# Optimization experiments

Hardware: AMD Instinct MI355X
Metric: run time of the kernel (lower is better)

Reference implementation:

```python
import jax, jax.numpy as jnp
import numpy as np

N, E, B, H, F = 20000, 400000, 200, 10, 78
HID = H * F  # 780
SEQ, VOC, EMB, NF, KS = 1000, 26, 128, 32, 8
CONV_OUT = SEQ - KS + 1  # 993


def setup_inputs() -> dict:
    key = jax.random.key(0)
    ks = jax.random.split(key, 40)
    g = lambda i, shape, s=0.05: jax.random.normal(ks[i], shape, jnp.float32) * s
    inp = {
        "x": jax.random.normal(ks[0], (N, F), jnp.float32),
        "edge_index": jax.random.randint(ks[1], (2, E), 0, N),
        "batch": jnp.sort(jax.random.randint(ks[2], (N,), 0, B)),
        "target": jax.random.randint(ks[3], (B, SEQ), 0, VOC),
        # GATConv(78 -> 78, heads=10)
        "gat_W": g(4, (F, HID)),
        "gat_a_src": g(5, (H, F)),
        "gat_a_dst": g(6, (H, F)),
        "gat_b": g(7, (HID,)),
        # GCNConv(780 -> 780)
        "gcn_W": g(8, (HID, HID)),
        "gcn_b": g(9, (HID,)),
        # graph MLP head
        "fcg1_W": g(10, (HID, 1500)), "fcg1_b": g(11, (1500,)),
        "fcg2_W": g(12, (1500, 128)), "fcg2_b": g(13, (128,)),
        # protein branch
        "emb": g(14, (VOC, EMB)),
        "cW": g(15, (NF, EMB, KS)), "cb": g(16, (NF,)),
        "fxt_W": g(17, (NF * CONV_OUT, 128)), "fxt_b": g(18, (128,)),
        # fusion MLP
        "f1_W": g(19, (256, 1024)), "f1_b": g(20, (1024,)),
        "f2_W": g(21, (1024, 512)), "f2_b": g(22, (512,)),
        "f3_W": g(23, (512, 256)), "f3_b": g(24, (256,)),
        "f4_W": g(25, (256, 128)), "f4_b": g(26, (128,)),
        "o_W": g(27, (128, 1)), "o_b": g(28, (1,)),
    }
    return inp


def _graph_branch(x, edge_index, batch, gat_W, gat_a_src, gat_a_dst, gat_b,
                  gcn_W, gcn_b, fcg1_W, fcg1_b, fcg2_W, fcg2_b):
    n = x.shape[0]
    loops = jnp.arange(n)
    src = jnp.concatenate([edge_index[0], loops])  # add self loops (PyG default)
    dst = jnp.concatenate([edge_index[1], loops])
    # --- GATConv ---
    h = (x @ gat_W).reshape(n, H, F)  # [N,H,F]
    a_s = jnp.einsum("nhf,hf->nh", h, gat_a_src)
    a_d = jnp.einsum("nhf,hf->nh", h, gat_a_dst)
    e = jax.nn.leaky_relu(a_s[src] + a_d[dst], 0.2)  # [Etot,H]
    m = jax.ops.segment_max(e, dst, num_segments=n)
    ex = jnp.exp(e - m[dst])
    den = jax.ops.segment_sum(ex, dst, num_segments=n)
    alpha = ex / den[dst]
    agg = jax.ops.segment_sum(h[src] * alpha[:, :, None], dst, num_segments=n)
    x1 = jax.nn.relu(agg.reshape(n, HID) + gat_b)
    # --- GCNConv (sym norm with self loops) ---
    deg = jax.ops.segment_sum(jnp.ones_like(dst, jnp.float32), dst, num_segments=n)
    dinv = jax.lax.rsqrt(jnp.maximum(deg, 1.0))
    norm = dinv[src] * dinv[dst]
    h2 = x1 @ gcn_W
    x2 = jax.ops.segment_sum(h2[src] * norm[:, None], dst, num_segments=n) + gcn_b
    x2 = jax.nn.relu(x2)
    # --- global add pool + MLP ---
    xg = jax.ops.segment_sum(x2, batch, num_segments=B)
    xg = jax.nn.relu(xg @ fcg1_W + fcg1_b)  # dropout = identity (eval)
    return xg @ fcg2_W + fcg2_b


def _protein_branch(target, emb, cW, cb, fxt_W, fxt_b):
    et = emb[target]  # [B,SEQ,EMB]
    c = jax.lax.conv_general_dilated(
        et.transpose(0, 2, 1), cW, (1,), "VALID",
        dimension_numbers=("NCH", "OIH", "NCH"))  # [B,NF,993]
    c = c + cb[None, :, None]
    return c.reshape(c.shape[0], NF * CONV_OUT) @ fxt_W + fxt_b


def reference(x, edge_index, batch, target, gat_W, gat_a_src, gat_a_dst, gat_b,
              gcn_W, gcn_b, fcg1_W, fcg1_b, fcg2_W, fcg2_b, emb, cW, cb,
              fxt_W, fxt_b, f1_W, f1_b, f2_W, f2_b, f3_W, f3_b, f4_W, f4_b,
              o_W, o_b):
    xg = _graph_branch(x, edge_index, batch, gat_W, gat_a_src, gat_a_dst, gat_b,
                       gcn_W, gcn_b, fcg1_W, fcg1_b, fcg2_W, fcg2_b)
    xt = _protein_branch(target, emb, cW, cb, fxt_W, fxt_b)
    xc = jnp.concatenate([xg, xt], axis=1)  # [B,256]
    xc = jax.nn.relu(xc @ f1_W + f1_b)
    xc = jax.nn.relu(xc @ f2_W + f2_b)
    xc = jax.nn.relu(xc @ f3_W + f3_b)
    xc = jax.nn.relu(xc @ f4_W + f4_b)
    return xc @ o_W + o_b  # [B,1]
```

## Files before the change

### kernel.cpp

```cpp
#include <hip/hip_runtime.h>
#include <hip/hip_bf16.h>
#include <math.h>

typedef __hip_bfloat16 bf16;
typedef __attribute__((ext_vector_type(8))) short short8v;
typedef __attribute__((ext_vector_type(4))) float float4v;

#define NODES 20000
#define EDG   400000
#define ETOT  (EDG + NODES)
#define GB    200
#define HEADS 10
#define FD    78
#define HIDD  780
#define SEQL  1000
#define VOCS  26
#define EMBD  128
#define NFC   32
#define KSZ   8
#define COUT  993
#define KFXT  (NFC * COUT)

#define MPAD  20096
#define NPADB 896
#define KP1   96
#define KP2   800
#define HP    784


__device__ __forceinline__ float us2f(unsigned short u) {
  unsigned int i = ((unsigned int)u) << 16; float f; __builtin_memcpy(&f, &i, 4); return f;
}
__device__ __forceinline__ float b2f(bf16 v) { return __bfloat162float(v); }
__device__ __forceinline__ float ldany(const void* p, size_t i, int m) {
  if (m) return ((const float*)p)[i];
  return b2f(((const bf16*)p)[i]);
}
__device__ __forceinline__ bool nanf_(float v) { return v != v; }
__device__ __forceinline__ unsigned short f2us(float v) {
  bf16 b = __float2bfloat16(v); unsigned short u; __builtin_memcpy(&u, &b, 2); return u;
}

__global__ void k_detect(const void* x, int* diag) {
  int t = threadIdx.x;
  const unsigned short* u = (const unsigned short*)x;
  int hit = 0;
  for (int i = t; i < 4096; i += 256) {
    float v = us2f(u[i]);
    if (nanf_(v) || fabsf(v) > 1e6f) hit = 1;
  }
  if (hit) diag[1] = 1;
}

__global__ void k_pad_x(const void* x, bf16* xpad, const int* diag) {
  int idx = blockIdx.x * 256 + threadIdx.x;
  if (idx >= MPAD * KP1) return;
  int mode = diag[1];
  int m = idx / KP1, k = idx % KP1;
  float v = (m < NODES && k < FD) ? ldany(x, (size_t)m * FD + k, mode) : 0.f;
  xpad[idx] = __float2bfloat16(v);
}

__global__ void k_tr_gatw(const void* gw, bf16* Wt, const int* diag) {
  int idx = blockIdx.x * 256 + threadIdx.x;
  if (idx >= NPADB * KP1) return;
  int mode = diag[1];
  int n = idx / KP1, k = idx % KP1;
  float v = (n < HIDD && k < FD) ? ldany(gw, (size_t)k * HIDD + n, mode) : 0.f;
  Wt[idx] = __float2bfloat16(v);
}

__global__ void k_tr_gcnw(const void* gw, bf16* Wt, const int* diag) {
  int idx = blockIdx.x * 256 + threadIdx.x;
  if (idx >= NPADB * KP2) return;
  int mode = diag[1];
  int n = idx / KP2, k = idx % KP2;
  float v = (n < HIDD && k < HIDD) ? ldany(gw, (size_t)k * HIDD + n, mode) : 0.f;
  Wt[idx] = __float2bfloat16(v);
}

__global__ void k_zero_x1pad(bf16* x1p) {
  int i = blockIdx.x * 256 + threadIdx.x;
  if (i < (MPAD - NODES) * KP2)
    x1p[(size_t)NODES * KP2 + i] = __float2bfloat16(0.f);
}

#define MT 128
#define NT 128
#define BK 32
#define LP 40
__global__ __launch_bounds__(256) void k_gemm_mfma(const bf16* A, int lda,
                                                   const bf16* Bt, int ldb,
                                                   bf16* C, int ldc, int Ncap,
                                                   int M, int Kp) {
  __shared__ __align__(16) bf16 As[MT * LP];
  __shared__ __align__(16) bf16 Bs[NT * LP];
  int t = threadIdx.x;
  int lane = t & 63, w = t >> 6;
  int wr = (w >> 1) * 64, wc = (w & 1) * 64;
  int quad = lane >> 4, mr = lane & 15;
  int m0 = blockIdx.y * MT, n0 = blockIdx.x * NT;
  float4v acc[4][4];
#pragma unroll
  for (int i = 0; i < 4; ++i)
#pragma unroll
    for (int j = 0; j < 4; ++j) acc[i][j] = (float4v){0.f, 0.f, 0.f, 0.f};

  for (int kc = 0; kc < Kp; kc += BK) {
#pragma unroll
    for (int i = 0; i < 4; ++i) {
      int c = t + i * 256;
      int row = c >> 3, col = (c & 7) * 4;
      *(uint2*)&As[row * LP + col] =
          *(const uint2*)&A[(size_t)(m0 + row) * lda + kc + col];
      *(uint2*)&Bs[row * LP + col] =
          *(const uint2*)&Bt[(size_t)(n0 + row) * ldb + kc + col];
    }
    __syncthreads();
    short8v af[4], bfr[4];
#pragma unroll
    for (int i = 0; i < 4; ++i)
      af[i] = *(const short8v*)&As[(wr + i * 16 + mr) * LP + quad * 8];
#pragma unroll
    for (int j = 0; j < 4; ++j)
      bfr[j] = *(const short8v*)&Bs[(wc + j * 16 + mr) * LP + quad * 8];
#pragma unroll
    for (int i = 0; i < 4; ++i)
#pragma unroll
      for (int j = 0; j < 4; ++j)
        acc[i][j] = __builtin_amdgcn_mfma_f32_16x16x32_bf16(af[i], bfr[j], acc[i][j], 0, 0, 0);
    __syncthreads();
  }
#pragma unroll
  for (int i = 0; i < 4; ++i) {
    int gm0 = m0 + wr + i * 16 + quad * 4;
#pragma unroll
    for (int j = 0; j < 4; ++j) {
      int gn = n0 + wc + j * 16 + mr;
      if (gn >= Ncap) continue;
#pragma unroll
      for (int r = 0; r < 4; ++r) {
        int gm = gm0 + r;
        if (gm < M) C[(size_t)gm * ldc + gn] = __float2bfloat16(acc[i][j][r]);
      }
    }
  }
}

#define MLP_NT 64
#define MLP_BK 32
#define MLP_MT 208
#define MLP_LP 40
__global__ __launch_bounds__(256) void k_mlp_mfma(const void* A, int lda, const void* Bw,
                                                  const void* bias, float* out, int ostride,
                                                  int ooff, int M, int Nn, int K,
                                                  int ksplit, int aRelu, int aBf16,
                                                  const int* diag) {
  __shared__ __align__(16) bf16 As[MLP_MT * MLP_LP];
  __shared__ __align__(16) bf16 Bs[MLP_NT * MLP_LP];
  int mode = diag[1];
  int t = threadIdx.x;
  int lane = t & 63, w = t >> 6;
  int quad = lane >> 4, mr = lane & 15;
  int n0 = blockIdx.x * MLP_NT;
  int kz = blockIdx.y;
  int nchunks = (K + MLP_BK - 1) / MLP_BK;
  int cpk = (nchunks + ksplit - 1) / ksplit;
  int c0 = kz * cpk, c1 = c0 + cpk;
  if (c1 > nchunks) c1 = nchunks;
  float4v acc[13];
#pragma unroll
  for (int i = 0; i < 13; ++i) acc[i] = (float4v){0.f, 0.f, 0.f, 0.f};

  for (int c = c0; c < c1; ++c) {
    int k0 = c * MLP_BK;
    if (aBf16) {
      const bf16* Ab = (const bf16*)A;
      for (int e = t; e < MLP_MT * 4; e += 256) {
        int row = e >> 2, c8 = (e & 3) * 8;
        int gk = k0 + c8;
        if (row < M && gk + 7 < K) {
          *(uint4*)&As[row * MLP_LP + c8] = *(const uint4*)&Ab[(size_t)row * lda + gk];
        } else {
#pragma unroll
          for (int kk = 0; kk < 8; ++kk) {
            float v = (row < M && gk + kk < K) ? b2f(Ab[(size_t)row * lda + gk + kk]) : 0.f;
            As[row * MLP_LP + c8 + kk] = __float2bfloat16(v);
          }
        }
      }
    } else {
      const float* Af = (const float*)A;
      for (int e = t; e < MLP_MT * 8; e += 256) {
        int row = e >> 3, c4 = (e & 7) * 4;
        int gk = k0 + c4;
        float4 v4 = {0.f, 0.f, 0.f, 0.f};
        if (row < M) {
          if (gk + 3 < K) {
            v4 = *(const float4*)&Af[(size_t)row * lda + gk];
          } else {
            v4.x = (gk + 0 < K) ? Af[(size_t)row * lda + gk + 0] : 0.f;
            v4.y = (gk + 1 < K) ? Af[(size_t)row * lda + gk + 1] : 0.f;
            v4.z = (gk + 2 < K) ? Af[(size_t)row * lda + gk + 2] : 0.f;
            v4.w = (gk + 3 < K) ? Af[(size_t)row * lda + gk + 3] : 0.f;
          }
        }
        if (aRelu) {
          v4.x = fmaxf(v4.x, 0.f); v4.y = fmaxf(v4.y, 0.f);
          v4.z = fmaxf(v4.z, 0.f); v4.w = fmaxf(v4.w, 0.f);
        }
        bf16* dst = &As[row * MLP_LP + c4];
        dst[0] = __float2bfloat16(v4.x); dst[1] = __float2bfloat16(v4.y);
        dst[2] = __float2bfloat16(v4.z); dst[3] = __float2bfloat16(v4.w);
      }
    }
    for (int e = t; e < MLP_NT * MLP_BK; e += 256) {
      int k = e >> 6, col = e & 63;
      int gk = k0 + k, gn = n0 + col;
      float v = (gn < Nn && gk < K) ? ldany(Bw, (size_t)gk * Nn + gn, mode) : 0.f;
      Bs[col * MLP_LP + k] = __float2bfloat16(v);
    }
    __syncthreads();
    short8v bf = *(const short8v*)&Bs[(w * 16 + mr) * MLP_LP + quad * 8];
#pragma unroll
    for (int i = 0; i < 13; ++i) {
      short8v af = *(const short8v*)&As[(i * 16 + mr) * MLP_LP + quad * 8];
      acc[i] = __builtin_amdgcn_mfma_f32_16x16x32_bf16(af, bf, acc[i], 0, 0, 0);
    }
    __syncthreads();
  }
  int gn = n0 + w * 16 + mr;
  if (gn >= Nn) return;
  float bs = (kz == 0) ? ldany(bias, gn, mode) : 0.f;
#pragma unroll
  for (int i = 0; i < 13; ++i) {
    int gm0 = i * 16 + quad * 4;
#pragma unroll
    for (int r = 0; r < 4; ++r) {
      int gm = gm0 + r;
      if (gm >= M) break;
      float v = acc[i][r] + bs;
      float* op = &out[(size_t)gm * ostride + ooff + gn];
      if (ksplit == 1) *op = v;
      else atomicAdd(op, v);
    }
  }
}

__global__ void k_prep_ws(const void* gat_W, const void* a_src, const void* a_dst,
                          float* Ws, float* Wd, const int* diag) {
  int idx = blockIdx.x * 256 + threadIdx.x;
  if (idx >= FD * HEADS) return;
  int mode = diag[1];
  int k = idx / HEADS, hd = idx % HEADS;
  float s = 0.f, d = 0.f;
  for (int f = 0; f < FD; ++f) {
    float w = ldany(gat_W, (size_t)k * HIDD + hd * FD + f, mode);
    s += w * ldany(a_src, (size_t)hd * FD + f, mode);
    d += w * ldany(a_dst, (size_t)hd * FD + f, mode);
  }
  Ws[k * HEADS + hd] = s;
  Wd[k * HEADS + hd] = d;
}

__global__ void k_prep_mtab(const void* emb, const void* cW, float* Mtab, const int* diag) {
  int idx = blockIdx.x * 256 + threadIdx.x;
  if (idx >= NFC * KSZ * VOCS) return;
  int mode = diag[1];
  int o = idx / (KSZ * VOCS);
  int r = idx % (KSZ * VOCS);
  int k = r / VOCS, v = r % VOCS;
  float acc = 0.f;
  for (int i = 0; i < EMBD; ++i)
    acc += ldany(emb, (size_t)v * EMBD + i, mode) * ldany(cW, ((size_t)o * EMBD + i) * KSZ + k, mode);
  Mtab[idx] = acc;
}

__global__ __launch_bounds__(256) void k_asd(const void* x, const float* Ws, const float* Wd,
                                             float* a_s, float* a_d, const int* diag) {
  __shared__ unsigned short xs[256 * FD];
  __shared__ float ws_sh[FD * HEADS], wd_sh[FD * HEADS];
  int mode = diag[1];
  int nb = blockIdx.x * 256, t = threadIdx.x;
  for (int e = t; e < FD * HEADS; e += 256) { ws_sh[e] = Ws[e]; wd_sh[e] = Wd[e]; }
  for (int e = t; e < 256 * FD; e += 256) {
    int r = e / FD, c = e % FD;
    int gn = nb + r;
    float xv = (gn < NODES) ? ldany(x, (size_t)gn * FD + c, mode) : 0.f;
    xs[e] = f2us(xv);
  }
  __syncthreads();
  int n = nb + t;
  if (n >= NODES) return;
  float as[HEADS], ad[HEADS];
#pragma unroll
  for (int hd = 0; hd < HEADS; ++hd) { as[hd] = 0.f; ad[hd] = 0.f; }
  for (int f = 0; f < FD; ++f) {
    float xv = us2f(xs[t * FD + f]);
#pragma unroll
    for (int hd = 0; hd < HEADS; ++hd) {
      as[hd] += xv * ws_sh[f * HEADS + hd];
      ad[hd] += xv * wd_sh[f * HEADS + hd];
    }
  }
#pragma unroll
  for (int hd = 0; hd < HEADS; ++hd) {
    a_s[n * HEADS + hd] = as[hd];
    a_d[n * HEADS + hd] = ad[hd];
  }
}

__global__ void k_count(const int* ei, int* cnt, int* diag) {
  int e = blockIdx.x * 256 + threadIdx.x;
  if (e >= ETOT) return;
  int d = (e < EDG) ? ei[EDG + e] : (e - EDG);
  if ((unsigned)d >= NODES) { atomicOr(diag, 8192); d = 0; }
  atomicAdd(&cnt[d], 1);
}

__global__ __launch_bounds__(1024) void k_scan(const int* cnt, int* rowstart) {
  __shared__ int sh[1024];
  __shared__ int carry;
  int t = threadIdx.x;
  if (t == 0) carry = 0;
  __syncthreads();
  for (int c = 0; c < (NODES + 1023) / 1024; ++c) {
    int i = c * 1024 + t;
    int v = (i < NODES) ? cnt[i] : 0;
    sh[t] = v;
    __syncthreads();
    for (int off = 1; off < 1024; off <<= 1) {
      int add = (t >= off) ? sh[t - off] : 0;
      __syncthreads();
      sh[t] += add;
      __syncthreads();
    }
    int tot = sh[1023];
    int excl = sh[t] - v + carry;
    if (i < NODES) rowstart[i] = excl;
    __syncthreads();
    if (t == 0) carry += tot;
    __syncthreads();
  }
  if (t == 0) rowstart[NODES] = carry;
}

__global__ void k_dinv(const int* cnt, float* dinv) {
  int n = blockIdx.x * 256 + threadIdx.x;
  if (n >= NODES) return;
  int d = cnt[n];
  dinv[n] = rsqrtf((float)(d > 0 ? d : 1));
}

__global__ void k_scatter(const int* ei, const int* rowstart, int* cur, int* es_src,
                          int* diag) {
  int e = blockIdx.x * 256 + threadIdx.x;
  if (e >= ETOT) return;
  int s, d;
  if (e < EDG) { s = ei[e]; d = ei[EDG + e]; } else { s = e - EDG; d = s; }
  if ((unsigned)d >= NODES) { atomicOr(diag, 8192); d = 0; }
  if ((unsigned)s >= NODES) { atomicOr(diag, 8192); s = 0; }
  int pos = rowstart[d] + atomicAdd(&cur[d], 1);
  if ((unsigned)pos < (unsigned)ETOT) es_src[pos] = s;
  else atomicOr(diag, 1);
}

__global__ void k_csrchk(const int* cnt, const int* cur, const int* rowst, int* diag) {
  int n = blockIdx.x * 256 + threadIdx.x;
  if (n < NODES && cur[n] != cnt[n]) atomicOr(diag, 1);
  if (n == 0 && rowst[NODES] != ETOT) atomicOr(diag, 1);
}

__global__ void k_bseg(const int* batch, int* bstart, int* diag) {
  int i = blockIdx.x * 256 + threadIdx.x;
  if (i >= NODES) return;
  int bi = batch[i];
  if ((unsigned)bi >= GB) { atomicOr(diag, 8192); bi = GB - 1; }
  int bp;
  if (i == 0) bp = -1;
  else {
    bp = batch[i - 1];
    if ((unsigned)bp >= GB) bp = GB - 1;
  }
  for (int b = bp + 1; b <= bi; ++b) bstart[b] = i;
  if (i == NODES - 1)
    for (int b = bi + 1; b <= GB; ++b) bstart[b] = NODES;
}

__global__ __launch_bounds__(256) void k_gat(const int* es_src, const int* rowstart,
                                             const float* a_s, const float* a_d,
                                             const bf16* h, const void* gat_b, bf16* x1,
                                             int* diag) {
  int d = blockIdx.x, t = threadIdx.x;
  __shared__ float ad_sh[HEADS], m_sh[HEADS], den_sh[HEADS];
  __shared__ float exs[256 * HEADS];
  __shared__ int ssrc[256];
  __shared__ float wred[4 * HEADS];
  int mode = diag[1];
  int start = rowstart[d], end = rowstart[d + 1];
  if (t < HEADS) ad_sh[t] = a_d[d * HEADS + t];
  __syncthreads();

  float mx[HEADS];
#pragma unroll
  for (int hd = 0; hd < HEADS; ++hd) mx[hd] = -INFINITY;
  for (int e = start + t; e < end; e += 256) {
    int s = es_src[e];
    if ((unsigned)s >= NODES) { atomicOr(diag, 1); s = 0; }
#pragma unroll
    for (int hd = 0; hd < HEADS; ++hd) {
      float v = a_s[s * HEADS + hd] + ad_sh[hd];
      v = v > 0.f ? v : 0.2f * v;
      mx[hd] = fmaxf(mx[hd], v);
    }
  }
#pragma unroll
  for (int hd = 0; hd < HEADS; ++hd)
    for (int off = 32; off; off >>= 1) mx[hd] = fmaxf(mx[hd], __shfl_down(mx[hd], off, 64));
  int w = t >> 6, lane = t & 63;
  if (lane == 0) {
#pragma unroll
    for (int hd = 0; hd < HEADS; ++hd) wred[w * HEADS + hd] = mx[hd];
  }
  __syncthreads();
  if (t < HEADS)
    m_sh[t] = fmaxf(fmaxf(wred[t], wred[HEADS + t]), fmaxf(wred[2 * HEADS + t], wred[3 * HEADS + t]));
  __syncthreads();

  float acc[4] = {0.f, 0.f, 0.f, 0.f};
  float den[HEADS];
#pragma unroll
  for (int hd = 0; hd < HEADS; ++hd) den[hd] = 0.f;
  int fb = t * 4;
  int hh[4];
#pragma unroll
  for (int k = 0; k < 4; ++k) {
    int f = fb + k;
    hh[k] = (f < HIDD) ? (f / FD) : (HEADS - 1);
  }
  for (int base = start; base < end; base += 256) {
    int ce = base + t;
    if (ce < end) {
      int s = es_src[ce];
      if ((unsigned)s >= NODES) { atomicOr(diag, 1); s = 0; }
      ssrc[t] = s;
#pragma unroll
      for (int hd = 0; hd < HEADS; ++hd) {
        float v = a_s[s * HEADS + hd] + ad_sh[hd];
        v = v > 0.f ? v : 0.2f * v;
        float ex = expf(v - m_sh[hd]);
        exs[t * HEADS + hd] = ex;
        den[hd] += ex;
      }
    }
    __syncthreads();
    int cnt2 = end - base; if (cnt2 > 256) cnt2 = 256;
    if (t < 196) {
      for (int ce2 = 0; ce2 < cnt2; ++ce2) {
        int ss = ssrc[ce2];
        uint2 u = *(const uint2*)(h + (size_t)ss * HP + fb);
        acc[0] += exs[ce2 * HEADS + hh[0]] * us2f((unsigned short)(u.x & 0xffffu));
        acc[1] += exs[ce2 * HEADS + hh[1]] * us2f((unsigned short)(u.x >> 16));
        acc[2] += exs[ce2 * HEADS + hh[2]] * us2f((unsigned short)(u.y & 0xffffu));
        acc[3] += exs[ce2 * HEADS + hh[3]] * us2f((unsigned short)(u.y >> 16));
      }
    }
    __syncthreads();
  }
#pragma unroll
  for (int hd = 0; hd < HEADS; ++hd)
    for (int off = 32; off; off >>= 1) den[hd] += __shfl_down(den[hd], off, 64);
  if (lane == 0) {
#pragma unroll
    for (int hd = 0; hd < HEADS; ++hd) wred[w * HEADS + hd] = den[hd];
  }
  __syncthreads();
  if (t < HEADS)
    den_sh[t] = wred[t] + wred[HEADS + t] + wred[2 * HEADS + t] + wred[3 * HEADS + t];
  __syncthreads();

  if (t < 196) {
    bool dn = nanf_(den_sh[hh[0]]) || nanf_(den_sh[hh[3]]);
    bool an = nanf_(acc[0]) || nanf_(acc[3]);
    if (dn) atomicOr(diag, 2);
    else if (an) atomicOr(diag, 8);
  }
  if (t < 200) {
    size_t rb = (size_t)d * KP2;
#pragma unroll
    for (int k = 0; k < 4; ++k) {
      int f = fb + k;
      float o = 0.f;
      if (f < HIDD)
        o = fmaxf(acc[k] / den_sh[hh[k]] + ldany(gat_b, f, mode), 0.f);
      x1[rb + f] = __float2bfloat16(o);
    }
  }
}

__global__ __launch_bounds__(256) void k_gcn(const int* es_src, const int* rowstart,
                                             const float* dinv, const bf16* h2,
                                             const void* gcn_b, bf16* x2b, int* diag) {
  int d = blockIdx.x, t = threadIdx.x;
  __shared__ float nrm[256];
  __shared__ int ssrc[256];
  int mode = diag[1];
  int start = rowstart[d], end = rowstart[d + 1];
  float dd = dinv[d];
  float acc[4] = {0.f, 0.f, 0.f, 0.f};
  int fb = t * 4;
  for (int base = start; base < end; base += 256) {
    int ce = base + t;
    if (ce < end) {
      int s = es_src[ce];
      if ((unsigned)s >= NODES) { atomicOr(diag, 1); s = 0; }
      ssrc[t] = s;
      nrm[t] = dinv[s] * dd;
    }
    __syncthreads();
    int cnt2 = end - base; if (cnt2 > 256) cnt2 = 256;
    if (t < 195) {
      for (int ce2 = 0; ce2 < cnt2; ++ce2) {
        int ss = ssrc[ce2];
        float nv = nrm[ce2];
        uint2 u = *(const uint2*)(h2 + (size_t)ss * HP + fb);
        acc[0] += nv * us2f((unsigned short)(u.x & 0xffffu));
        acc[1] += nv * us2f((unsigned short)(u.x >> 16));
        acc[2] += nv * us2f((unsigned short)(u.y & 0xffffu));
        acc[3] += nv * us2f((unsigned short)(u.y >> 16));
      }
    }
    __syncthreads();
  }
  if (t < 196) {
    if (t < 195 && (nanf_(acc[0]) || nanf_(acc[3]))) atomicOr(diag, 16);
    unsigned short o[4];
#pragma unroll
    for (int k = 0; k < 4; ++k) {
      int f = fb + k;
      float v = 0.f;
      if (f < HIDD) v = fmaxf(acc[k] + ldany(gcn_b, f, mode), 0.f);
      o[k] = f2us(v);
    }
    uint2 pack;
    __builtin_memcpy(&pack, o, 8);
    *(uint2*)(x2b + (size_t)d * HP + fb) = pack;
  }
}

__global__ __launch_bounds__(256) void k_pool(const bf16* x2b, const int* bstart,
                                              float* xg_pool) {
  int b = blockIdx.x, t = threadIdx.x;
  if (t >= 195) return;
  int r0 = bstart[b], r1 = bstart[b + 1];
  int fb = t * 4;
  float4 acc = {0.f, 0.f, 0.f, 0.f};
  for (int r = r0; r < r1; ++r) {
    uint2 u = *(const uint2*)(x2b + (size_t)r * HP + fb);
    acc.x += us2f((unsigned short)(u.x & 0xffffu));
    acc.y += us2f((unsigned short)(u.x >> 16));
    acc.z += us2f((unsigned short)(u.y & 0xffffu));
    acc.w += us2f((unsigned short)(u.y >> 16));
  }
  *(float4*)&xg_pool[(size_t)b * HIDD + fb] = acc;
}

__global__ __launch_bounds__(256) void k_conv(const int* target, const float* Mtab,
                                              const void* cb, bf16* c, int* diag) {
  int b = blockIdx.y, tc = blockIdx.x, t = threadIdx.x;
  __shared__ float Mt[NFC * KSZ * VOCS];
  __shared__ int tg[256 + KSZ - 1];
  int mode = diag[1];
  for (int e = t; e < NFC * KSZ * VOCS; e += 256) Mt[e] = Mtab[e];
  int tbase = tc * 256;
  for (int e = t; e < 256 + KSZ - 1; e += 256) {
    int p = tbase + e;
    int tv = (p < SEQL) ? target[b * SEQL + p] : 0;
    if ((unsigned)tv >= VOCS) { atomicOr(diag, 8192); tv = 0; }
    tg[e] = tv;
  }
  __syncthreads();
  int tt = tbase + t;
  if (tt >= COUT) return;
  float acc[NFC];
#pragma unroll
  for (int o = 0; o < NFC; ++o) acc[o] = 0.f;
#pragma unroll
  for (int k = 0; k < KSZ; ++k) {
    int v = tg[t + k];
    const float* Mk = &Mt[k * VOCS + v];
#pragma unroll
    for (int o = 0; o < NFC; ++o) acc[o] += Mk[o * KSZ * VOCS];
  }
  if (nanf_(acc[0])) atomicOr(diag, 4096);
#pragma unroll
  for (int o = 0; o < NFC; ++o)
    c[(size_t)b * KFXT + o * COUT + tt] = __float2bfloat16(acc[o] + ldany(cb, o, mode));
}

__global__ __launch_bounds__(64) void k_out(const float* xf4, const void* o_W,
                                            const void* o_b, void* outp, const int* diag) {
  int b = blockIdx.x, lane = threadIdx.x;
  int mode = diag[1];
  float a0 = fmaxf(xf4[b * 128 + lane], 0.f);
  float a1 = fmaxf(xf4[b * 128 + 64 + lane], 0.f);
  float v = a0 * ldany(o_W, lane, mode) + a1 * ldany(o_W, 64 + lane, mode);
  for (int off = 32; off; off >>= 1) v += __shfl_down(v, off, 64);
  if (lane == 0) {
    float r = v + ldany(o_b, 0, mode);
    int dg = diag[0];
    if (dg) r = 256.f * (1 + mode) + 8.f * (float)(__ffs(dg) - 1);
    else if (nanf_(r)) r = 200.f + 100.f * mode;
    if (mode) ((float*)outp)[b] = r;
    else ((bf16*)outp)[b] = __float2bfloat16(r);
  }
}

extern "C" void kernel_launch(void* const* d_in, const int* in_sizes, int n_in,
                              void* d_out, int out_size, void* d_ws, size_t ws_size,
                              hipStream_t stream) {
  const void* x       = d_in[0];
  const int*  ei      = (const int*)d_in[1];
  const int*  batch   = (const int*)d_in[2];
  const int*  target  = (const int*)d_in[3];
  const void* gat_W   = d_in[4];
  const void* a_src   = d_in[5];
  const void* a_dst   = d_in[6];
  const void* gat_b   = d_in[7];
  const void* gcn_W   = d_in[8];
  const void* gcn_b   = d_in[9];
  const void* fcg1_W  = d_in[10];
  const void* fcg1_b  = d_in[11];
  const void* fcg2_W  = d_in[12];
  const void* fcg2_b  = d_in[13];
  const void* emb     = d_in[14];
  const void* cW      = d_in[15];
  const void* cb      = d_in[16];
  const void* fxt_W   = d_in[17];
  const void* fxt_b   = d_in[18];
  const void* f1_W    = d_in[19];
  const void* f1_b    = d_in[20];
  const void* f2_W    = d_in[21];
  const void* f2_b    = d_in[22];
  const void* f3_W    = d_in[23];
  const void* f3_b    = d_in[24];
  const void* f4_W    = d_in[25];
  const void* f4_b    = d_in[26];
  const void* o_W     = d_in[27];
  const void* o_b     = d_in[28];

  char* w = (char*)d_ws;
  size_t off = 0;
  auto alloc = [&](size_t bytes) -> void* {
    void* p = w + off;
    off = (off + bytes + 255) & ~(size_t)255;
    return p;
  };
  bf16*  h_buf   = (bf16*)alloc((size_t)NODES * HP * 2);
  bf16*  x1p     = (bf16*)alloc((size_t)MPAD * KP2 * 2);
  bf16*  xpad    = (bf16*)alloc((size_t)MPAD * KP1 * 2);
  bf16*  gatWt   = (bf16*)alloc((size_t)NPADB * KP1 * 2);
  bf16*  gcnWt   = (bf16*)alloc((size_t)NPADB * KP2 * 2);
  float* a_s     = (float*)alloc((size_t)NODES * HEADS * 4);
  float* a_d     = (float*)alloc((size_t)NODES * HEADS * 4);
  float* Ws      = (float*)alloc(FD * HEADS * 4);
  float* Wd      = (float*)alloc(FD * HEADS * 4);
  float* Mtab    = (float*)alloc(NFC * KSZ * VOCS * 4);
  int*   rowst   = (int*)alloc((NODES + 1) * 4);
  float* dinv    = (float*)alloc(NODES * 4);
  int*   bstart  = (int*)alloc((GB + 1) * 4);
  bf16*  c_buf   = (bf16*)alloc((size_t)GB * KFXT * 2);
  size_t zoff = off;
  int*   cnt     = (int*)alloc(NODES * 4);
  int*   cur     = (int*)alloc(NODES * 4);
  int*   es_src  = (int*)alloc((size_t)ETOT * 4);
  float* xg_pool = (float*)alloc((size_t)GB * HIDD * 4);
  float* xg1     = (float*)alloc((size_t)GB * 1500 * 4);
  float* xc      = (float*)alloc((size_t)GB * 256 * 4);
  float* xf1     = (float*)alloc((size_t)GB * 1024 * 4);
  float* xf2     = (float*)alloc((size_t)GB * 512 * 4);
  float* xf3     = (float*)alloc((size_t)GB * 256 * 4);
  float* xf4     = (float*)alloc((size_t)GB * 128 * 4);
  int*   diag    = (int*)alloc(2 * 4);
  size_t zlen = off - zoff;

  bf16* x2b = x1p;

  hipMemsetAsync(w + zoff, 0, zlen, stream);

  k_detect<<<1, 256, 0, stream>>>(x, diag);

  k_pad_x<<<(MPAD * KP1 + 255) / 256, 256, 0, stream>>>(x, xpad, diag);
  k_tr_gatw<<<(NPADB * KP1 + 255) / 256, 256, 0, stream>>>(gat_W, gatWt, diag);
  k_tr_gcnw<<<(NPADB * KP2 + 255) / 256, 256, 0, stream>>>(gcn_W, gcnWt, diag);
  k_zero_x1pad<<<((MPAD - NODES) * KP2 + 255) / 256, 256, 0, stream>>>(x1p);

  k_prep_ws<<<(FD * HEADS + 255) / 256, 256, 0, stream>>>(gat_W, a_src, a_dst, Ws, Wd, diag);
  k_prep_mtab<<<(NFC * KSZ * VOCS + 255) / 256, 256, 0, stream>>>(emb, cW, Mtab, diag);

  k_gemm_mfma<<<dim3(NPADB / NT, MPAD / MT), 256, 0, stream>>>(
      xpad, KP1, gatWt, KP1, h_buf, HP, HP, NODES, KP1);
  k_asd<<<(NODES + 255) / 256, 256, 0, stream>>>(x, Ws, Wd, a_s, a_d, diag);

  k_count<<<(ETOT + 255) / 256, 256, 0, stream>>>(ei, cnt, diag);
  k_scan<<<1, 1024, 0, stream>>>(cnt, rowst);
  k_dinv<<<(NODES + 255) / 256, 256, 0, stream>>>(cnt, dinv);
  k_scatter<<<(ETOT + 255) / 256, 256, 0, stream>>>(ei, rowst, cur, es_src, diag);
  k_csrchk<<<(NODES + 255) / 256, 256, 0, stream>>>(cnt, cur, rowst, diag);
  k_bseg<<<(NODES + 255) / 256, 256, 0, stream>>>(batch, bstart, diag);

  k_gat<<<NODES, 256, 0, stream>>>(es_src, rowst, a_s, a_d, h_buf, gat_b, x1p, diag);

  k_gemm_mfma<<<dim3(NPADB / NT, MPAD / MT), 256, 0, stream>>>(
      x1p, KP2, gcnWt, KP2, h_buf, HP, HP, NODES, KP2);

  k_gcn<<<NODES, 256, 0, stream>>>(es_src, rowst, dinv, h_buf, gcn_b, x2b, diag);
  k_pool<<<GB, 256, 0, stream>>>(x2b, bstart, xg_pool);

  k_conv<<<dim3(4, GB), 256, 0, stream>>>(target, Mtab, cb, c_buf, diag);

  k_mlp_mfma<<<dim3(24, 4), 256, 0, stream>>>(xg_pool, HIDD, fcg1_W, fcg1_b,
                                              xg1, 1500, 0, GB, 1500, HIDD, 4, 0, 0, diag);
  k_mlp_mfma<<<dim3(2, 16), 256, 0, stream>>>(xg1, 1500, fcg2_W, fcg2_b,
                                              xc, 256, 0, GB, 128, 1500, 16, 1, 0, diag);
  k_mlp_mfma<<<dim3(2, 64), 256, 0, stream>>>(c_buf, KFXT, fxt_W, fxt_b,
                                              xc, 256, 128, GB, 128, KFXT, 64, 0, 1, diag);
  k_mlp_mfma<<<dim3(16, 4), 256, 0, stream>>>(xc, 256, f1_W, f1_b,
                                              xf1, 1024, 0, GB, 1024, 256, 4, 0, 0, diag);
  k_mlp_mfma<<<dim3(8, 8), 256, 0, stream>>>(xf1, 1024, f2_W, f2_b,
                                             xf2, 512, 0, GB, 512, 1024, 8, 1, 0, diag);
  k_mlp_mfma<<<dim3(4, 8), 256, 0, stream>>>(xf2, 512, f3_W, f3_b,
                                             xf3, 256, 0, GB, 256, 512, 8, 1, 0, diag);
  k_mlp_mfma<<<dim3(2, 8), 256, 0, stream>>>(xf3, 256, f4_W, f4_b,
                                             xf4, 128, 0, GB, 128, 256, 8, 1, 0, diag);
  k_out<<<GB, 64, 0, stream>>>(xf4, o_W, o_b, d_out, diag);
}
```

Before: 0.9996 ms.

## Split GAT into alpha pass and feature-panelled gather kernels

```diff
diff --git a/kernel.cpp b/kernel.cpp
--- a/kernel.cpp
+++ b/kernel.cpp
@@ -25,7 +25,9 @@
 #define NPADB 896
 #define KP1   96
 #define KP2   800
-#define HP    784
+#define HP    800
+#define PNL   8
+#define PF    100
 
 
 __device__ __forceinline__ float us2f(unsigned short u) {
@@ -387,142 +389,156 @@
     for (int b = bi + 1; b <= GB; ++b) bstart[b] = NODES;
 }
 
-__global__ __launch_bounds__(256) void k_gat(const int* es_src, const int* rowstart,
-                                             const float* a_s, const float* a_d,
-                                             const bf16* h, const void* gat_b, bf16* x1,
-                                             int* diag) {
-  int d = blockIdx.x, t = threadIdx.x;
-  __shared__ float ad_sh[HEADS], m_sh[HEADS], den_sh[HEADS];
-  __shared__ float exs[256 * HEADS];
-  __shared__ int ssrc[256];
-  __shared__ float wred[4 * HEADS];
-  int mode = diag[1];
-  int start = rowstart[d], end = rowstart[d + 1];
-  if (t < HEADS) ad_sh[t] = a_d[d * HEADS + t];
-  __syncthreads();
-
+__global__ __launch_bounds__(64) void k_alpha(const int* es_src, const int* rowst,
+                                              const float* a_s, const float* a_d,
+                                              float* alpha, int* diag) {
+  int d = blockIdx.x, lane = threadIdx.x;
+  int start = rowst[d], end = rowst[d + 1];
+  float ad[HEADS];
+#pragma unroll
+  for (int j = 0; j < HEADS; ++j) ad[j] = a_d[d * HEADS + j];
   float mx[HEADS];
 #pragma unroll
-  for (int hd = 0; hd < HEADS; ++hd) mx[hd] = -INFINITY;
-  for (int e = start + t; e < end; e += 256) {
-    int s = es_src[e];
-    if ((unsigned)s >= NODES) { atomicOr(diag, 1); s = 0; }
-#pragma unroll
-    for (int hd = 0; hd < HEADS; ++hd) {
-      float v = a_s[s * HEADS + hd] + ad_sh[hd];
-      v = v > 0.f ? v : 0.2f * v;
-      mx[hd] = fmaxf(mx[hd], v);
-    }
-  }
-#pragma unroll
-  for (int hd = 0; hd < HEADS; ++hd)
-    for (int off = 32; off; off >>= 1) mx[hd] = fmaxf(mx[hd], __shfl_down(mx[hd], off, 64));
-  int w = t >> 6, lane = t & 63;
-  if (lane == 0) {
-#pragma unroll
-    for (int hd = 0; hd < HEADS; ++hd) wred[w * HEADS + hd] = mx[hd];
-  }
-  __syncthreads();
-  if (t < HEADS)
-    m_sh[t] = fmaxf(fmaxf(wred[t], wred[HEADS + t]), fmaxf(wred[2 * HEADS + t], wred[3 * HEADS + t]));
-  __syncthreads();
-
-  float acc[4] = {0.f, 0.f, 0.f, 0.f};
-  float den[HEADS];
-#pragma unroll
-  for (int hd = 0; hd < HEADS; ++hd) den[hd] = 0.f;
-  int fb = t * 4;
-  int hh[4];
-#pragma unroll
-  for (int k = 0; k < 4; ++k) {
-    int f = fb + k;
-    hh[k] = (f < HIDD) ? (f / FD) : (HEADS - 1);
-  }
-  for (int base = start; base < end; base += 256) {
-    int ce = base + t;
+  for (int j = 0; j < HEADS; ++j) mx[j] = -INFINITY;
+  for (int base = start; base < end; base += 64) {
+    int ce = base + lane;
     if (ce < end) {
       int s = es_src[ce];
       if ((unsigned)s >= NODES) { atomicOr(diag, 1); s = 0; }
-      ssrc[t] = s;
-#pragma unroll
-      for (int hd = 0; hd < HEADS; ++hd) {
-        float v = a_s[s * HEADS + hd] + ad_sh[hd];
+#pragma unroll
+      for (int j = 0; j < HEADS; ++j) {
+        float v = a_s[s * HEADS + j] + ad[j];
         v = v > 0.f ? v : 0.2f * v;
-        float ex = expf(v - m_sh[hd]);
-        exs[t * HEADS + hd] = ex;
-        den[hd] += ex;
+        mx[j] = fmaxf(mx[j], v);
       }
     }
-    __syncthreads();
-    int cnt2 = end - base; if (cnt2 > 256) cnt2 = 256;
-    if (t < 196) {
-      for (int ce2 = 0; ce2 < cnt2; ++ce2) {
-        int ss = ssrc[ce2];
-        uint2 u = *(const uint2*)(h + (size_t)ss * HP + fb);
-        acc[0] += exs[ce2 * HEADS + hh[0]] * us2f((unsigned short)(u.x & 0xffffu));
-        acc[1] += exs[ce2 * HEADS + hh[1]] * us2f((unsigned short)(u.x >> 16));
-        acc[2] += exs[ce2 * HEADS + hh[2]] * us2f((unsigned short)(u.y & 0xffffu));
-        acc[3] += exs[ce2 * HEADS + hh[3]] * us2f((unsigned short)(u.y >> 16));
+  }
+#pragma unroll
+  for (int j = 0; j < HEADS; ++j)
+    for (int off = 1; off < 64; off <<= 1) mx[j] = fmaxf(mx[j], __shfl_xor(mx[j], off, 64));
+  float den[HEADS];
+#pragma unroll
+  for (int j = 0; j < HEADS; ++j) den[j] = 0.f;
+  for (int base = start; base < end; base += 64) {
+    int ce = base + lane;
+    if (ce < end) {
+      int s = es_src[ce];
+      if ((unsigned)s >= NODES) s = 0;
+#pragma unroll
+      for (int j = 0; j < HEADS; ++j) {
+        float v = a_s[s * HEADS + j] + ad[j];
+        v = v > 0.f ? v : 0.2f * v;
+        den[j] += expf(v - mx[j]);
       }
     }
-    __syncthreads();
-  }
-#pragma unroll
-  for (int hd = 0; hd < HEADS; ++hd)
-    for (int off = 32; off; off >>= 1) den[hd] += __shfl_down(den[hd], off, 64);
-  if (lane == 0) {
-#pragma unroll
-    for (int hd = 0; hd < HEADS; ++hd) wred[w * HEADS + hd] = den[hd];
-  }
-  __syncthreads();
-  if (t < HEADS)
-    den_sh[t] = wred[t] + wred[HEADS + t] + wred[2 * HEADS + t] + wred[3 * HEADS + t];
-  __syncthreads();
-
-  if (t < 196) {
-    bool dn = nanf_(den_sh[hh[0]]) || nanf_(den_sh[hh[3]]);
-    bool an = nanf_(acc[0]) || nanf_(acc[3]);
-    if (dn) atomicOr(diag, 2);
-    else if (an) atomicOr(diag, 8);
-  }
-  if (t < 200) {
-    size_t rb = (size_t)d * KP2;
-#pragma unroll
-    for (int k = 0; k < 4; ++k) {
-      int f = fb + k;
-      float o = 0.f;
-      if (f < HIDD)
-        o = fmaxf(acc[k] / den_sh[hh[k]] + ldany(gat_b, f, mode), 0.f);
-      x1[rb + f] = __float2bfloat16(o);
-    }
-  }
-}
-
-__global__ __launch_bounds__(256) void k_gcn(const int* es_src, const int* rowstart,
-                                             const float* dinv, const bf16* h2,
-                                             const void* gcn_b, bf16* x2b, int* diag) {
-  int d = blockIdx.x, t = threadIdx.x;
-  __shared__ float nrm[256];
-  __shared__ int ssrc[256];
-  int mode = diag[1];
-  int start = rowstart[d], end = rowstart[d + 1];
-  float dd = dinv[d];
+  }
+#pragma unroll
+  for (int j = 0; j < HEADS; ++j)
+    for (int off = 1; off < 64; off <<= 1) den[j] += __shfl_xor(den[j], off, 64);
+  if (lane == 0 && (nanf_(den[0]) || nanf_(den[HEADS - 1]))) atomicOr(diag, 2);
+  for (int base = start; base < end; base += 64) {
+    int ce = base + lane;
+    if (ce < end) {
+      int s = es_src[ce];
+      if ((unsigned)s >= NODES) s = 0;
+#pragma unroll
+      for (int j = 0; j < HEADS; ++j) {
+        float v = a_s[s * HEADS + j] + ad[j];
+        v = v > 0.f ? v : 0.2f * v;
+        alpha[(size_t)ce * HEADS + j] = expf(v - mx[j]) / den[j];
+      }
+    }
+  }
+}
+
+__global__ __launch_bounds__(64) void k_gatg(const int* es_src, const int* rowst,
+                                             const float* alpha, const bf16* h,
+                                             const void* gat_b, bf16* x1, int* diag) {
+  __shared__ int ssc[64];
+  __shared__ float alw[64 * HEADS];
+  int bid = blockIdx.x;
+  int p = bid & (PNL - 1), d = bid >> 3;
+  int lane = threadIdx.x;
+  int mode = diag[1];
+  int start = rowst[d], end = rowst[d + 1];
+  int fb = p * PF + lane * 4;
+  int hA = fb / FD; if (hA > HEADS - 1) hA = HEADS - 1;
+  int hB = (fb + 3) / FD; if (hB > HEADS - 1) hB = HEADS - 1;
+  bool selB[4];
+#pragma unroll
+  for (int k = 0; k < 4; ++k) {
+    int hk = (fb + k) / FD; if (hk > HEADS - 1) hk = HEADS - 1;
+    selB[k] = (hk != hA);
+  }
   float acc[4] = {0.f, 0.f, 0.f, 0.f};
-  int fb = t * 4;
-  for (int base = start; base < end; base += 256) {
-    int ce = base + t;
+  for (int base = start; base < end; base += 64) {
+    int ce = base + lane;
     if (ce < end) {
       int s = es_src[ce];
       if ((unsigned)s >= NODES) { atomicOr(diag, 1); s = 0; }
-      ssrc[t] = s;
-      nrm[t] = dinv[s] * dd;
-    }
-    __syncthreads();
-    int cnt2 = end - base; if (cnt2 > 256) cnt2 = 256;
-    if (t < 195) {
-      for (int ce2 = 0; ce2 < cnt2; ++ce2) {
-        int ss = ssrc[ce2];
-        float nv = nrm[ce2];
+      ssc[lane] = s;
+#pragma unroll
+      for (int j = 0; j < HEADS; ++j) alw[lane * HEADS + j] = alpha[(size_t)ce * HEADS + j];
+    }
+    __syncthreads();
+    int cnt2 = end - base; if (cnt2 > 64) cnt2 = 64;
+    if (lane < 25) {
+      for (int e = 0; e < cnt2; ++e) {
+        int ss = ssc[e];
+        float aA = alw[e * HEADS + hA];
+        float aB = alw[e * HEADS + hB];
+        uint2 u = *(const uint2*)(h + (size_t)ss * HP + fb);
+        acc[0] += (selB[0] ? aB : aA) * us2f((unsigned short)(u.x & 0xffffu));
+        acc[1] += (selB[1] ? aB : aA) * us2f((unsigned short)(u.x >> 16));
+        acc[2] += (selB[2] ? aB : aA) * us2f((unsigned short)(u.y & 0xffffu));
+        acc[3] += (selB[3] ? aB : aA) * us2f((unsigned short)(u.y >> 16));
+      }
+    }
+    __syncthreads();
+  }
+  if (lane < 25) {
+    if (nanf_(acc[0]) || nanf_(acc[3])) atomicOr(diag, 8);
+    unsigned short o[4];
+#pragma unroll
+    for (int k = 0; k < 4; ++k) {
+      int f = fb + k;
+      float v = 0.f;
+      if (f < HIDD) v = fmaxf(acc[k] + ldany(gat_b, f, mode), 0.f);
+      o[k] = f2us(v);
+    }
+    uint2 pack;
+    __builtin_memcpy(&pack, o, 8);
+    *(uint2*)(x1 + (size_t)d * KP2 + fb) = pack;
+  }
+}
+
+__global__ __launch_bounds__(64) void k_gcng(const int* es_src, const int* rowst,
+                                             const float* dinv, const bf16* h2,
+                                             const void* gcn_b, bf16* x2b, int* diag) {
+  __shared__ int ssc[64];
+  __shared__ float nw[64];
+  int bid = blockIdx.x;
+  int p = bid & (PNL - 1), d = bid >> 3;
+  int lane = threadIdx.x;
+  int mode = diag[1];
+  int start = rowst[d], end = rowst[d + 1];
+  float dd = dinv[d];
+  int fb = p * PF + lane * 4;
+  float acc[4] = {0.f, 0.f, 0.f, 0.f};
+  for (int base = start; base < end; base += 64) {
+    int ce = base + lane;
+    if (ce < end) {
+      int s = es_src[ce];
+      if ((unsigned)s >= NODES) { atomicOr(diag, 1); s = 0; }
+      ssc[lane] = s;
+      nw[lane] = dinv[s] * dd;
+    }
+    __syncthreads();
+    int cnt2 = end - base; if (cnt2 > 64) cnt2 = 64;
+    if (lane < 25) {
+      for (int e = 0; e < cnt2; ++e) {
+        int ss = ssc[e];
+        float nv = nw[e];
         uint2 u = *(const uint2*)(h2 + (size_t)ss * HP + fb);
         acc[0] += nv * us2f((unsigned short)(u.x & 0xffffu));
         acc[1] += nv * us2f((unsigned short)(u.x >> 16));
@@ -532,8 +548,8 @@
     }
     __syncthreads();
   }
-  if (t < 196) {
-    if (t < 195 && (nanf_(acc[0]) || nanf_(acc[3]))) atomicOr(diag, 16);
+  if (lane < 25) {
+    if (nanf_(acc[0]) || nanf_(acc[3])) atomicOr(diag, 16);
     unsigned short o[4];
 #pragma unroll
     for (int k = 0; k < 4; ++k) {
@@ -663,6 +679,7 @@
   bf16*  gcnWt   = (bf16*)alloc((size_t)NPADB * KP2 * 2);
   float* a_s     = (float*)alloc((size_t)NODES * HEADS * 4);
   float* a_d     = (float*)alloc((size_t)NODES * HEADS * 4);
+  float* alpha   = (float*)alloc((size_t)ETOT * HEADS * 4);
   float* Ws      = (float*)alloc(FD * HEADS * 4);
   float* Wd      = (float*)alloc(FD * HEADS * 4);
   float* Mtab    = (float*)alloc(NFC * KSZ * VOCS * 4);
@@ -709,12 +726,13 @@
   k_csrchk<<<(NODES + 255) / 256, 256, 0, stream>>>(cnt, cur, rowst, diag);
   k_bseg<<<(NODES + 255) / 256, 256, 0, stream>>>(batch, bstart, diag);
 
-  k_gat<<<NODES, 256, 0, stream>>>(es_src, rowst, a_s, a_d, h_buf, gat_b, x1p, diag);
+  k_alpha<<<NODES, 64, 0, stream>>>(es_src, rowst, a_s, a_d, alpha, diag);
+  k_gatg<<<NODES * PNL, 64, 0, stream>>>(es_src, rowst, alpha, h_buf, gat_b, x1p, diag);
 
   k_gemm_mfma<<<dim3(NPADB / NT, MPAD / MT), 256, 0, stream>>>(
       x1p, KP2, gcnWt, KP2, h_buf, HP, HP, NODES, KP2);
 
-  k_gcn<<<NODES, 256, 0, stream>>>(es_src, rowst, dinv, h_buf, gcn_b, x2b, diag);
+  k_gcng<<<NODES * PNL, 64, 0, stream>>>(es_src, rowst, dinv, h_buf, gcn_b, x2b, diag);
   k_pool<<<GB, 256, 0, stream>>>(x2b, bstart, xg_pool);
 
   k_conv<<<dim3(4, GB), 256, 0, stream>>>(target, Mtab, cb, c_buf, diag);
```

New measurement: 1.023 ms. 1.02x slower.
